# Kernel optimization log

Measured on AMD Instinct MI355X. Metric: run time of the kernel, lower is better.

The kernel has to match this reference:

```python
import jax, jax.numpy as jnp
import numpy as np

K0, K1 = 3, 3  # kernel_size
UNITS = K0 * K1


def setup_inputs() -> dict:
    key = jax.random.key(0)
    k1, k2, k3 = jax.random.split(key, 3)
    B, S = 100, 512  # batch fixed to 100 by the original code's np.zeros((100,1)) pad
    inputs = jax.random.normal(k1, (B, S, S, 1), dtype=jnp.float32)
    # per-position unshared weights/bias, 'random_normal' initializer (stddev 0.05)
    w = jax.random.normal(k2, (S * S * UNITS,), dtype=jnp.float32) * 0.05
    b = jax.random.normal(k3, (S * S * UNITS,), dtype=jnp.float32) * 0.05
    return {"inputs": inputs, "w": w, "b": b}


def reference(inputs, w, b):
    # Faithful to the original (including its quirks):
    #  - taps read diagonal entries inputs[:, j+t, j+t] for t in [0, UNITS)
    #    (tmp_j is never reset across the m loop)
    #  - validity mask uses (tmp_i = i + t//K1, tmp_j = j + t)
    #  - bias b is added BEFORE reduce_sum over units, so
    #    out[b,i,j] = UNITS * dot(v, w_ij) + sum(b_ij)
    B, W, H, C = inputs.shape  # C == 1, W == H
    t = jnp.arange(UNITS)
    diag = inputs[:, jnp.arange(H), jnp.arange(H), 0]          # (B, H)
    jj = jnp.arange(H)[:, None] + t[None, :]                   # (H, UNITS) tmp_j
    valid_j = jj < H
    gathered = jnp.where(valid_j[None], diag[:, jnp.minimum(jj, H - 1)], 0.0)  # (B,H,UNITS)
    ii = jnp.arange(W)[:, None] + (t // K1)[None, :]           # (W, UNITS) tmp_i
    valid_i = (ii < W).astype(inputs.dtype)
    w3 = w.reshape(W, H, UNITS) * valid_i[:, None, :]          # mask taps by tmp_i bound
    dot = jnp.einsum('bjt,ijt->bij', gathered, w3)             # (B, W, H)
    bias = b.reshape(W, H, UNITS).sum(-1)                      # (W, H)
    out = UNITS * dot + bias[None]
    return out.reshape(B, W * H)  # position order: i * tmp_h + j
```

## Files before the change

kernel.cpp:

```cpp
#include <hip/hip_runtime.h>

#define S 512
#define UNITS 9
#define IPB 4
#define RPT 8
#define BLOCK 256
#define BCHUNK 10

__global__ void diag_extract_kernel(const float* __restrict__ in,
                                    float* __restrict__ diag, int BS) {
    int idx = blockIdx.x * blockDim.x + threadIdx.x;
    if (idx < BS) {
        int b = idx >> 9;
        int j = idx & (S - 1);
        diag[idx] = in[(size_t)b * S * S + (size_t)j * (S + 1)];
    }
}

__global__ __launch_bounds__(BLOCK, 4) void cnn_main_kernel(
        const float* __restrict__ w, const float* __restrict__ bv,
        const float* __restrict__ diag, const float* __restrict__ raw_in,
        float* __restrict__ out, int B) {
    __shared__ __align__(16) float sdiag[S + 8];

    const int group = blockIdx.x & ((S / IPB) - 1);
    const int chunk = blockIdx.x / (S / IPB);
    const int row   = threadIdx.x >> 6;
    const int lane  = threadIdx.x & 63;
    const int i     = group * IPB + row;
    const int j0    = lane * RPT;

    float wv[RPT * UNITS];
    {
        const float4* ws4 = reinterpret_cast<const float4*>(
            w + (size_t)(i * S + j0) * UNITS);
        #pragma unroll
        for (int q = 0; q < RPT * UNITS / 4; ++q) {
            float4 v = ws4[q];
            wv[4*q+0] = v.x; wv[4*q+1] = v.y; wv[4*q+2] = v.z; wv[4*q+3] = v.w;
        }
    }
    if (i >= S - 2) {
        const int tmax = (i == S - 1) ? 3 : 6;
        #pragma unroll
        for (int k = 0; k < RPT * UNITS; ++k)
            if ((k % UNITS) >= tmax) wv[k] = 0.f;
    }

    float bias[RPT];
    {
        float bb[RPT * UNITS];
        const float4* bs4 = reinterpret_cast<const float4*>(
            bv + (size_t)(i * S + j0) * UNITS);
        #pragma unroll
        for (int q = 0; q < RPT * UNITS / 4; ++q) {
            float4 v = bs4[q];
            bb[4*q+0] = v.x; bb[4*q+1] = v.y; bb[4*q+2] = v.z; bb[4*q+3] = v.w;
        }
        #pragma unroll
        for (int r = 0; r < RPT; ++r) {
            float s = 0.f;
            #pragma unroll
            for (int t = 0; t < UNITS; ++t) s += bb[r * UNITS + t];
            bias[r] = s;
        }
    }

    const int b0 = chunk * BCHUNK;
    for (int bb = 0; bb < BCHUNK; ++bb) {
        const int b = b0 + bb;
        if (b >= B) break;

        __syncthreads();
        for (int idx = threadIdx.x; idx < S + 8; idx += BLOCK) {
            float v = 0.f;
            if (idx < S)
                v = diag ? diag[(size_t)b * S + idx]
                         : raw_in[(size_t)b * S * S + (size_t)idx * (S + 1)];
            sdiag[idx] = v;
        }
        __syncthreads();

        float dv[RPT + UNITS - 1];
        const float4* d4 = reinterpret_cast<const float4*>(&sdiag[j0]);
        #pragma unroll
        for (int q = 0; q < 4; ++q) {
            float4 v = d4[q];
            dv[4*q+0] = v.x; dv[4*q+1] = v.y; dv[4*q+2] = v.z; dv[4*q+3] = v.w;
        }

        float res[RPT];
        #pragma unroll
        for (int r = 0; r < RPT; ++r) {
            float acc = 0.f;
            #pragma unroll
            for (int t = 0; t < UNITS; ++t)
                acc = fmaf(dv[r + t], wv[r * UNITS + t], acc);
            res[r] = fmaf(acc, (float)UNITS, bias[r]);
        }

        float4* o4 = reinterpret_cast<float4*>(
            out + (size_t)b * S * S + (size_t)i * S + j0);
        o4[0] = make_float4(res[0], res[1], res[2], res[3]);
        o4[1] = make_float4(res[4], res[5], res[6], res[7]);
    }
}

extern "C" void kernel_launch(void* const* d_in, const int* in_sizes, int n_in,
                              void* d_out, int out_size, void* d_ws, size_t ws_size,
                              hipStream_t stream) {
    const float* in = (const float*)d_in[0];
    const float* w  = (const float*)d_in[1];
    const float* bv = (const float*)d_in[2];
    float* out      = (float*)d_out;

    const int B  = in_sizes[0] / (S * S);
    const int BS = B * S;

    float* diag = nullptr;
    if (ws_size >= (size_t)BS * sizeof(float)) {
        diag = (float*)d_ws;
        diag_extract_kernel<<<(BS + 255) / 256, 256, 0, stream>>>(in, diag, BS);
    }

    const int nchunk = (B + BCHUNK - 1) / BCHUNK;
    dim3 grid((S / IPB) * nchunk);
    cnn_main_kernel<<<grid, BLOCK, 0, stream>>>(w, bv, diag, in, out, B);
}
```

Measured before the change: 217.8 us.

## Read padded diagonal directly from workspace and split each thread's columns into two coalesced halves

The diagonal workspace is padded to 520 entries per batch so the main kernel can read it straight from global memory (cached) instead of staging it through shared memory with two barriers per batch. Each thread now handles two groups of four columns, at j=4*lane and j=256+4*lane, so a wavefront's weight, bias and output accesses are contiguous float4 strips rather than 8-wide strided chunks. The minimum-occupancy hint is removed from launch bounds. The risk is that dropping the occupancy hint may raise register use and lower occupancy, and per-thread global diagonal loads rely on cache hits.

Result: faster. 207.3 us (-4.8%).

```diff
diff --git a/kernel.cpp b/kernel.cpp
--- a/kernel.cpp
+++ b/kernel.cpp
@@ -1,67 +1,74 @@
 #include <hip/hip_runtime.h>
 
 #define S 512
+#define SP 520
 #define UNITS 9
-#define IPB 4
-#define RPT 8
 #define BLOCK 256
 #define BCHUNK 10
 
 __global__ void diag_extract_kernel(const float* __restrict__ in,
-                                    float* __restrict__ diag, int BS) {
+                                    float* __restrict__ diag, int B) {
     int idx = blockIdx.x * blockDim.x + threadIdx.x;
-    if (idx < BS) {
-        int b = idx >> 9;
-        int j = idx & (S - 1);
-        diag[idx] = in[(size_t)b * S * S + (size_t)j * (S + 1)];
+    if (idx < B * SP) {
+        int b = idx / SP;
+        int j = idx - b * SP;
+        diag[idx] = (j < S) ? in[(size_t)b * S * S + (size_t)j * (S + 1)] : 0.f;
     }
 }
 
-__global__ __launch_bounds__(BLOCK, 4) void cnn_main_kernel(
+template<bool USE_WS>
+__global__ __launch_bounds__(BLOCK) void cnn_main_kernel(
         const float* __restrict__ w, const float* __restrict__ bv,
         const float* __restrict__ diag, const float* __restrict__ raw_in,
         float* __restrict__ out, int B) {
-    __shared__ __align__(16) float sdiag[S + 8];
+    __shared__ __align__(16) float sdiag[USE_WS ? 1 : SP];
 
-    const int group = blockIdx.x & ((S / IPB) - 1);
-    const int chunk = blockIdx.x / (S / IPB);
+    const int group = blockIdx.x & ((S / 4) - 1);
+    const int chunk = blockIdx.x >> 7;
     const int row   = threadIdx.x >> 6;
     const int lane  = threadIdx.x & 63;
-    const int i     = group * IPB + row;
-    const int j0    = lane * RPT;
+    const int i     = group * 4 + row;
+    const int jA    = 4 * lane;
+    const int jB    = 256 + 4 * lane;
 
-    float wv[RPT * UNITS];
+    float wv[72];
     {
-        const float4* ws4 = reinterpret_cast<const float4*>(
-            w + (size_t)(i * S + j0) * UNITS);
+        const float4* wa = reinterpret_cast<const float4*>(w + (size_t)(i * S + jA) * UNITS);
+        const float4* wb = reinterpret_cast<const float4*>(w + (size_t)(i * S + jB) * UNITS);
         #pragma unroll
-        for (int q = 0; q < RPT * UNITS / 4; ++q) {
-            float4 v = ws4[q];
-            wv[4*q+0] = v.x; wv[4*q+1] = v.y; wv[4*q+2] = v.z; wv[4*q+3] = v.w;
+        for (int q = 0; q < 9; ++q) {
+            float4 va = wa[q], vb = wb[q];
+            wv[4*q+0] = va.x; wv[4*q+1] = va.y; wv[4*q+2] = va.z; wv[4*q+3] = va.w;
+            wv[36+4*q+0] = vb.x; wv[36+4*q+1] = vb.y; wv[36+4*q+2] = vb.z; wv[36+4*q+3] = vb.w;
         }
     }
     if (i >= S - 2) {
         const int tmax = (i == S - 1) ? 3 : 6;
         #pragma unroll
-        for (int k = 0; k < RPT * UNITS; ++k)
-            if ((k % UNITS) >= tmax) wv[k] = 0.f;
+        for (int h = 0; h < 2; ++h)
+            #pragma unroll
+            for (int r = 0; r < 4; ++r)
+                #pragma unroll
+                for (int t = 0; t < UNITS; ++t)
+                    if (t >= tmax) wv[36*h + r*UNITS + t] = 0.f;
     }
 
-    float bias[RPT];
+    float bias[8];
     {
-        float bb[RPT * UNITS];
-        const float4* bs4 = reinterpret_cast<const float4*>(
-            bv + (size_t)(i * S + j0) * UNITS);
+        float tmp[72];
+        const float4* ba = reinterpret_cast<const float4*>(bv + (size_t)(i * S + jA) * UNITS);
+        const float4* bb = reinterpret_cast<const float4*>(bv + (size_t)(i * S + jB) * UNITS);
         #pragma unroll
-        for (int q = 0; q < RPT * UNITS / 4; ++q) {
-            float4 v = bs4[q];
-            bb[4*q+0] = v.x; bb[4*q+1] = v.y; bb[4*q+2] = v.z; bb[4*q+3] = v.w;
+        for (int q = 0; q < 9; ++q) {
+            float4 va = ba[q], vb = bb[q];
+            tmp[4*q+0] = va.x; tmp[4*q+1] = va.y; tmp[4*q+2] = va.z; tmp[4*q+3] = va.w;
+            tmp[36+4*q+0] = vb.x; tmp[36+4*q+1] = vb.y; tmp[36+4*q+2] = vb.z; tmp[36+4*q+3] = vb.w;
         }
         #pragma unroll
-        for (int r = 0; r < RPT; ++r) {
+        for (int r = 0; r < 8; ++r) {
             float s = 0.f;
             #pragma unroll
-            for (int t = 0; t < UNITS; ++t) s += bb[r * UNITS + t];
+            for (int t = 0; t < UNITS; ++t) s += tmp[r * UNITS + t];
             bias[r] = s;
         }
     }
@@ -71,38 +78,46 @@
         const int b = b0 + bb;
         if (b >= B) break;
 
-        __syncthreads();
-        for (int idx = threadIdx.x; idx < S + 8; idx += BLOCK) {
-            float v = 0.f;
-            if (idx < S)
-                v = diag ? diag[(size_t)b * S + idx]
-                         : raw_in[(size_t)b * S * S + (size_t)idx * (S + 1)];
-            sdiag[idx] = v;
-        }
-        __syncthreads();
-
-        float dv[RPT + UNITS - 1];
-        const float4* d4 = reinterpret_cast<const float4*>(&sdiag[j0]);
-        #pragma unroll
-        for (int q = 0; q < 4; ++q) {
-            float4 v = d4[q];
-            dv[4*q+0] = v.x; dv[4*q+1] = v.y; dv[4*q+2] = v.z; dv[4*q+3] = v.w;
+        const float* p;
+        if (USE_WS) {
+            p = diag + (size_t)b * SP;
+        } else {
+            __syncthreads();
+            for (int idx = threadIdx.x; idx < SP; idx += BLOCK)
+                sdiag[idx] = (idx < S) ? raw_in[(size_t)b * S * S + (size_t)idx * (S + 1)] : 0.f;
+            __syncthreads();
+            p = sdiag;
         }
 
-        float res[RPT];
-        #pragma unroll
-        for (int r = 0; r < RPT; ++r) {
-            float acc = 0.f;
+        float dA[12], dB[12];
+        {
+            const float4* pa = reinterpret_cast<const float4*>(p + jA);
+            const float4* pb = reinterpret_cast<const float4*>(p + jB);
             #pragma unroll
-            for (int t = 0; t < UNITS; ++t)
-                acc = fmaf(dv[r + t], wv[r * UNITS + t], acc);
-            res[r] = fmaf(acc, (float)UNITS, bias[r]);
+            for (int q = 0; q < 3; ++q) {
+                float4 va = pa[q], vb = pb[q];
+                dA[4*q+0] = va.x; dA[4*q+1] = va.y; dA[4*q+2] = va.z; dA[4*q+3] = va.w;
+                dB[4*q+0] = vb.x; dB[4*q+1] = vb.y; dB[4*q+2] = vb.z; dB[4*q+3] = vb.w;
+            }
         }
 
-        float4* o4 = reinterpret_cast<float4*>(
-            out + (size_t)b * S * S + (size_t)i * S + j0);
-        o4[0] = make_float4(res[0], res[1], res[2], res[3]);
-        o4[1] = make_float4(res[4], res[5], res[6], res[7]);
+        float4 resA, resB;
+        float* rA = &resA.x; float* rB = &resB.x;
+        #pragma unroll
+        for (int r = 0; r < 4; ++r) {
+            float accA = 0.f, accB = 0.f;
+            #pragma unroll
+            for (int t = 0; t < UNITS; ++t) {
+                accA = fmaf(dA[r + t], wv[r * UNITS + t], accA);
+                accB = fmaf(dB[r + t], wv[36 + r * UNITS + t], accB);
+            }
+            rA[r] = fmaf(accA, (float)UNITS, bias[r]);
+            rB[r] = fmaf(accB, (float)UNITS, bias[4 + r]);
+        }
+
+        float* orow = out + (size_t)b * S * S + (size_t)i * S;
+        *reinterpret_cast<float4*>(orow + jA) = resA;
+        *reinterpret_cast<float4*>(orow + jB) = resB;
     }
 }
 
@@ -114,16 +129,15 @@
     const float* bv = (const float*)d_in[2];
     float* out      = (float*)d_out;
 
-    const int B  = in_sizes[0] / (S * S);
-    const int BS = B * S;
+    const int B = in_sizes[0] / (S * S);
+    const int nchunk = (B + BCHUNK - 1) / BCHUNK;
+    dim3 grid((S / 4) * nchunk);
 
-    float* diag = nullptr;
-    if (ws_size >= (size_t)BS * sizeof(float)) {
-        diag = (float*)d_ws;
-        diag_extract_kernel<<<(BS + 255) / 256, 256, 0, stream>>>(in, diag, BS);
+    if (ws_size >= (size_t)B * SP * sizeof(float)) {
+        float* diag = (float*)d_ws;
+        diag_extract_kernel<<<(B * SP + 255) / 256, 256, 0, stream>>>(in, diag, B);
+        cnn_main_kernel<true><<<grid, BLOCK, 0, stream>>>(w, bv, diag, in, out, B);
+    } else {
+        cnn_main_kernel<false><<<grid, BLOCK, 0, stream>>>(w, bv, nullptr, in, out, B);
     }
-
-    const int nchunk = (B + BCHUNK - 1) / BCHUNK;
-    dim3 grid((S / IPB) * nchunk);
-    cnn_main_kernel<<<grid, BLOCK, 0, stream>>>(w, bv, diag, in, out, B);
 }
```
